# Kernel optimization log

Hardware: AMD Instinct MI355X
Metric: run time of the kernel (lower is better)

## Reference

```python
import jax, jax.numpy as jnp
import numpy as np

WIN_H = 3
WIN_W = 3
DILATION = 1
CUT = 0.0  # module hard-codes self.cut = 0
EPS = 1e-12  # torch F.normalize eps


def _l2norm(x):
    # L2-normalize over channel dim (dim=1), matching torch.nn.functional.normalize
    n = jnp.sqrt(jnp.sum(x * x, axis=1, keepdims=True))
    return x / jnp.maximum(n, EPS)


def setup_inputs() -> dict:
    key = jax.random.key(0)
    k1, k2 = jax.random.split(key)
    B, C, H, W = 4, 128, 192, 256
    image = jax.random.normal(k1, (B, C, H, W), dtype=jnp.float32)
    event = jax.random.normal(k2, (B, C, H, W), dtype=jnp.float32)
    return {"image": image, "event": event}


def reference(image, event):
    B, C, H, W = image.shape
    img = _l2norm(image)
    evt = _l2norm(event)
    p = DILATION
    imgp = jnp.pad(img, ((0, 0), (0, 0), (p, p), (p, p)))
    evtp = jnp.pad(evt, ((0, 0), (0, 0), (p, p), (p, p)))
    # Unfold ordering: reshape(B, C, K, H, W) with K positions row-major over (i, j).
    # affinity_k(p) = sum_c img_shift_k(p) * evt_shift_k(p)  -> avoid im2col blowup,
    # compute per-offset shifted dot products instead.
    affs = []
    for i in range(WIN_H):
        for j in range(WIN_W):
            oi, oj = i * DILATION, j * DILATION
            a = jnp.sum(
                imgp[:, :, oi:oi + H, oj:oj + W] * evtp[:, :, oi:oi + H, oj:oj + W],
                axis=1,
            )  # [B, H, W]
            affs.append(a)
    affinity = jnp.stack(affs, axis=1)  # [B, K=9, H, W]
    # affinity[affinity < cut] = cut  with cut == 0
    return jnp.maximum(affinity, CUT)
```

## Files before the change

### kernel.cpp

```cpp
#include <hip/hip_runtime.h>

#define BB 4
#define CC 128
#define HH 192
#define WW 256
#define HW (HH * WW)

__global__ __launch_bounds__(256) void dotnorm_kernel(
    const float* __restrict__ img, const float* __restrict__ evt,
    float* __restrict__ D)
{
    const int row = blockIdx.x;
    const int tid = threadIdx.x;
    const int qx  = tid & 63;
    const int cz  = tid >> 6;
    const int b   = row / HH;
    const int h   = row - b * HH;
    const int w0  = qx << 2;
    const int base0 = b * CC * HW + h * WW + w0;
    const int c0  = cz * 32;

    float4 aii = make_float4(0.f, 0.f, 0.f, 0.f);
    float4 aee = make_float4(0.f, 0.f, 0.f, 0.f);
    float4 aie = make_float4(0.f, 0.f, 0.f, 0.f);

    #pragma unroll 8
    for (int c = 0; c < 32; ++c) {
        const float4 iv = *reinterpret_cast<const float4*>(img + base0 + (c0 + c) * HW);
        const float4 ev = *reinterpret_cast<const float4*>(evt + base0 + (c0 + c) * HW);
        aii.x += iv.x * iv.x; aii.y += iv.y * iv.y; aii.z += iv.z * iv.z; aii.w += iv.w * iv.w;
        aee.x += ev.x * ev.x; aee.y += ev.y * ev.y; aee.z += ev.z * ev.z; aee.w += ev.w * ev.w;
        aie.x += iv.x * ev.x; aie.y += iv.y * ev.y; aie.z += iv.z * ev.z; aie.w += iv.w * ev.w;
    }

    __shared__ float s_ii[4][256];
    __shared__ float s_ee[4][256];
    __shared__ float s_ie[4][256];
    const int p4 = qx << 2;
    s_ii[cz][p4 + 0] = aii.x; s_ii[cz][p4 + 1] = aii.y; s_ii[cz][p4 + 2] = aii.z; s_ii[cz][p4 + 3] = aii.w;
    s_ee[cz][p4 + 0] = aee.x; s_ee[cz][p4 + 1] = aee.y; s_ee[cz][p4 + 2] = aee.z; s_ee[cz][p4 + 3] = aee.w;
    s_ie[cz][p4 + 0] = aie.x; s_ie[cz][p4 + 1] = aie.y; s_ie[cz][p4 + 2] = aie.z; s_ie[cz][p4 + 3] = aie.w;
    __syncthreads();

    const float ii = s_ii[0][tid] + s_ii[1][tid] + s_ii[2][tid] + s_ii[3][tid];
    const float ee = s_ee[0][tid] + s_ee[1][tid] + s_ee[2][tid] + s_ee[3][tid];
    const float ie = s_ie[0][tid] + s_ie[1][tid] + s_ie[2][tid] + s_ie[3][tid];
    const float ni = fmaxf(sqrtf(ii), 1e-12f);
    const float ne = fmaxf(sqrtf(ee), 1e-12f);
    D[row * WW + tid] = ie / (ni * ne);
}

__global__ __launch_bounds__(256) void gather_kernel(
    const float* __restrict__ D, float* __restrict__ out)
{
    const int idx = blockIdx.x * 256 + threadIdx.x;
    const int qx  = idx & 63;
    const int rh  = idx >> 6;
    const int b   = rh / HH;
    const int h   = rh - b * HH;
    const int w0  = qx << 2;

    float r[3][6];
    #pragma unroll
    for (int dy = 0; dy < 3; ++dy) {
        const int y = h + dy - 1;
        const bool vy = (y >= 0) && (y < HH);
        const int rowbase = (b * HH + y) * WW;
        #pragma unroll
        for (int x = 0; x < 6; ++x) {
            const int xx = w0 + x - 1;
            r[dy][x] = (vy && xx >= 0 && xx < WW) ? D[rowbase + xx] : 0.0f;
        }
    }

    #pragma unroll
    for (int i = 0; i < 3; ++i) {
        #pragma unroll
        for (int j = 0; j < 3; ++j) {
            float4 o;
            o.x = fmaxf(r[i][j + 0], 0.0f);
            o.y = fmaxf(r[i][j + 1], 0.0f);
            o.z = fmaxf(r[i][j + 2], 0.0f);
            o.w = fmaxf(r[i][j + 3], 0.0f);
            const int k = i * 3 + j;
            *reinterpret_cast<float4*>(out + (((b * 9 + k) * HH + h) * WW + w0)) = o;
        }
    }
}

extern "C" void kernel_launch(void* const* d_in, const int* in_sizes, int n_in,
                              void* d_out, int out_size, void* d_ws, size_t ws_size,
                              hipStream_t stream) {
    const float* img = (const float*)d_in[0];
    const float* evt = (const float*)d_in[1];
    float* out = (float*)d_out;
    float* D   = (float*)d_ws;

    dotnorm_kernel<<<BB * HH, 256, 0, stream>>>(img, evt, D);
    gather_kernel<<<(BB * HH * WW / 4) / 256, 256, 0, stream>>>(D, out);
}
```

Baseline: 43.18 us.

## Split channel reduction across more blocks and map gather threads to output

The dot/norm kernel now splits each row into four 64-pixel segments, each handled by its own block of 256 threads covering 16 channel groups of 8. This quadruples the grid and shortens each thread's serial load chain, raising memory-level parallelism over the large input read. The gather kernel now assigns one thread per output float4 of a single offset, making stores fully linear. The cost is redundant reads of D across offsets and a heavier shared-memory reduction done by only 64 threads.

After: 38.86 us. 10.0% less time.

```diff
diff --git a/kernel.cpp b/kernel.cpp
--- a/kernel.cpp
+++ b/kernel.cpp
@@ -10,82 +10,81 @@
     const float* __restrict__ img, const float* __restrict__ evt,
     float* __restrict__ D)
 {
-    const int row = blockIdx.x;
+    const int blk = blockIdx.x;
     const int tid = threadIdx.x;
-    const int qx  = tid & 63;
-    const int cz  = tid >> 6;
+    const int qx  = tid & 15;
+    const int cz  = tid >> 4;
+    const int seg = blk & 3;
+    const int row = blk >> 2;
     const int b   = row / HH;
     const int h   = row - b * HH;
-    const int w0  = qx << 2;
+    const int w0  = seg * 64 + (qx << 2);
     const int base0 = b * CC * HW + h * WW + w0;
-    const int c0  = cz * 32;
+    const int cbase = cz * 8;
 
     float4 aii = make_float4(0.f, 0.f, 0.f, 0.f);
     float4 aee = make_float4(0.f, 0.f, 0.f, 0.f);
     float4 aie = make_float4(0.f, 0.f, 0.f, 0.f);
 
-    #pragma unroll 8
-    for (int c = 0; c < 32; ++c) {
-        const float4 iv = *reinterpret_cast<const float4*>(img + base0 + (c0 + c) * HW);
-        const float4 ev = *reinterpret_cast<const float4*>(evt + base0 + (c0 + c) * HW);
+    #pragma unroll
+    for (int c = 0; c < 8; ++c) {
+        const float4 iv = *reinterpret_cast<const float4*>(img + base0 + (cbase + c) * HW);
+        const float4 ev = *reinterpret_cast<const float4*>(evt + base0 + (cbase + c) * HW);
         aii.x += iv.x * iv.x; aii.y += iv.y * iv.y; aii.z += iv.z * iv.z; aii.w += iv.w * iv.w;
         aee.x += ev.x * ev.x; aee.y += ev.y * ev.y; aee.z += ev.z * ev.z; aee.w += ev.w * ev.w;
         aie.x += iv.x * ev.x; aie.y += iv.y * ev.y; aie.z += iv.z * ev.z; aie.w += iv.w * ev.w;
     }
 
-    __shared__ float s_ii[4][256];
-    __shared__ float s_ee[4][256];
-    __shared__ float s_ie[4][256];
+    __shared__ float s_ii[16][64];
+    __shared__ float s_ee[16][64];
+    __shared__ float s_ie[16][64];
     const int p4 = qx << 2;
     s_ii[cz][p4 + 0] = aii.x; s_ii[cz][p4 + 1] = aii.y; s_ii[cz][p4 + 2] = aii.z; s_ii[cz][p4 + 3] = aii.w;
     s_ee[cz][p4 + 0] = aee.x; s_ee[cz][p4 + 1] = aee.y; s_ee[cz][p4 + 2] = aee.z; s_ee[cz][p4 + 3] = aee.w;
     s_ie[cz][p4 + 0] = aie.x; s_ie[cz][p4 + 1] = aie.y; s_ie[cz][p4 + 2] = aie.z; s_ie[cz][p4 + 3] = aie.w;
     __syncthreads();
 
-    const float ii = s_ii[0][tid] + s_ii[1][tid] + s_ii[2][tid] + s_ii[3][tid];
-    const float ee = s_ee[0][tid] + s_ee[1][tid] + s_ee[2][tid] + s_ee[3][tid];
-    const float ie = s_ie[0][tid] + s_ie[1][tid] + s_ie[2][tid] + s_ie[3][tid];
-    const float ni = fmaxf(sqrtf(ii), 1e-12f);
-    const float ne = fmaxf(sqrtf(ee), 1e-12f);
-    D[row * WW + tid] = ie / (ni * ne);
+    if (tid < 64) {
+        float ii = 0.f, ee = 0.f, ie = 0.f;
+        #pragma unroll
+        for (int k = 0; k < 16; ++k) {
+            ii += s_ii[k][tid];
+            ee += s_ee[k][tid];
+            ie += s_ie[k][tid];
+        }
+        const float ni = fmaxf(sqrtf(ii), 1e-12f);
+        const float ne = fmaxf(sqrtf(ee), 1e-12f);
+        D[row * WW + seg * 64 + tid] = ie / (ni * ne);
+    }
 }
 
 __global__ __launch_bounds__(256) void gather_kernel(
     const float* __restrict__ D, float* __restrict__ out)
 {
     const int idx = blockIdx.x * 256 + threadIdx.x;
-    const int qx  = idx & 63;
-    const int rh  = idx >> 6;
-    const int b   = rh / HH;
-    const int h   = rh - b * HH;
-    const int w0  = qx << 2;
+    const int qx   = idx & 63;
+    const int rest = idx >> 6;
+    const int h    = rest % HH;
+    const int bk   = rest / HH;
+    const int k    = bk % 9;
+    const int b    = bk / 9;
+    const int i    = k / 3;
+    const int j    = k - 3 * i;
+    const int w0   = qx << 2;
 
-    float r[3][6];
+    const int y  = h + i - 1;
+    const bool vy = (y >= 0) && (y < HH);
+    const int rowbase = (b * HH + y) * WW;
+
+    float4 o;
+    float* op = &o.x;
     #pragma unroll
-    for (int dy = 0; dy < 3; ++dy) {
-        const int y = h + dy - 1;
-        const bool vy = (y >= 0) && (y < HH);
-        const int rowbase = (b * HH + y) * WW;
-        #pragma unroll
-        for (int x = 0; x < 6; ++x) {
-            const int xx = w0 + x - 1;
-            r[dy][x] = (vy && xx >= 0 && xx < WW) ? D[rowbase + xx] : 0.0f;
-        }
+    for (int e = 0; e < 4; ++e) {
+        const int x = w0 + e + j - 1;
+        const float v = (vy && x >= 0 && x < WW) ? D[rowbase + x] : 0.0f;
+        op[e] = fmaxf(v, 0.0f);
     }
-
-    #pragma unroll
-    for (int i = 0; i < 3; ++i) {
-        #pragma unroll
-        for (int j = 0; j < 3; ++j) {
-            float4 o;
-            o.x = fmaxf(r[i][j + 0], 0.0f);
-            o.y = fmaxf(r[i][j + 1], 0.0f);
-            o.z = fmaxf(r[i][j + 2], 0.0f);
-            o.w = fmaxf(r[i][j + 3], 0.0f);
-            const int k = i * 3 + j;
-            *reinterpret_cast<float4*>(out + (((b * 9 + k) * HH + h) * WW + w0)) = o;
-        }
-    }
+    *reinterpret_cast<float4*>(out + (size_t)idx * 4) = o;
 }
 
 extern "C" void kernel_launch(void* const* d_in, const int* in_sizes, int n_in,
@@ -96,6 +95,6 @@
     float* out = (float*)d_out;
     float* D   = (float*)d_ws;
 
-    dotnorm_kernel<<<BB * HH, 256, 0, stream>>>(img, evt, D);
-    gather_kernel<<<(BB * HH * WW / 4) / 256, 256, 0, stream>>>(D, out);
+    dotnorm_kernel<<<BB * HH * 4, 256, 0, stream>>>(img, evt, D);
+    gather_kernel<<<(BB * 9 * HH * WW / 4) / 256, 256, 0, stream>>>(D, out);
 }
```
